# Kernel tuning notes

Measured on AMD Instinct MI355X. Metric: run time of the kernel, lower is better.

The kernel has to match this reference:

```python
import jax, jax.numpy as jnp
import numpy as np

# dims: S slots, B batch, D pred-rep dim, E slot-embedding dim, H hidden/output dim, V per-slot vocab
S, B, D, E, H, V = 7, 4096, 1024, 128, 512, 200
D0 = D + E  # layer-0 LSTM input size


def setup_inputs() -> dict:
    key = jax.random.key(0)
    ks = jax.random.split(key, 12)
    rn = lambda k, shape, s=0.02: jax.random.normal(k, shape, jnp.float32) * s
    return {
        "pred_reps": jax.random.normal(ks[0], (B, D), jnp.float32),
        "slot_labels": jax.random.randint(ks[1], (S, B), 0, V),
        "emb": rn(ks[2], (S, V, E), 1.0),
        # layer 0: per-slot LSTMCell + highway params
        "Wih0": rn(ks[3], (S, 4 * H, D0)), "Whh0": rn(ks[4], (S, 4 * H, H)),
        "bih0": jnp.zeros((S, 4 * H), jnp.float32), "bhh0": jnp.zeros((S, 4 * H), jnp.float32),
        "hwW0": rn(ks[5], (S, H, D0 + H)), "hwb0": jnp.zeros((S, H), jnp.float32),
        "linW0": rn(ks[6], (S, H, D0)),
        # layer 1 (input size = H)
        "Wih1": rn(ks[7], (S, 4 * H, H)), "Whh1": rn(ks[8], (S, 4 * H, H)),
        "bih1": jnp.zeros((S, 4 * H), jnp.float32), "bhh1": jnp.zeros((S, 4 * H), jnp.float32),
        "hwW1": rn(ks[9], (S, H, 2 * H)), "hwb1": jnp.zeros((S, H), jnp.float32),
        "linW1": rn(ks[10], (S, H, H)),
    }


def _lstm_cell(x, h, c, Wih, Whh, bih, bhh):
    # torch LSTMCell: gates ordered i, f, g, o
    gates = x @ Wih.T + bih + h @ Whh.T + bhh
    i, f, g, o = jnp.split(gates, 4, axis=-1)
    c_new = jax.nn.sigmoid(f) * c + jax.nn.sigmoid(i) * jnp.tanh(g)
    h_new = jax.nn.sigmoid(o) * jnp.tanh(c_new)
    return h_new, c_new


def reference(pred_reps, slot_labels, emb, Wih0, Whh0, bih0, bhh0, hwW0, hwb0, linW0,
              Wih1, Whh1, bih1, bhh1, hwW1, hwb1, linW1):
    def step(carry, xs):
        h0, c0, h1, c1 = carry
        (tbl, idx, wih0, whh0, bi0, bh0, hw0, hb0, lw0,
         wih1, whh1, bi1, bh1, hw1, hb1, lw1) = xs
        # per-slot embedding gather + concat with predicate reps  -> [B, D0]
        x = jnp.concatenate([pred_reps, tbl[idx]], axis=-1)
        # layer 0 cell + highway gate
        h0n, c0n = _lstm_cell(x, h0, c0, wih0, whh0, bi0, bh0)
        gate0 = jax.nn.sigmoid(jnp.concatenate([x, h0n], axis=-1) @ hw0.T + hb0)
        x1 = gate0 * h0n + (1.0 - gate0) * (x @ lw0.T)
        # layer 1 cell (its highway output is dead code in the original: curr_input
        # after the last layer is discarded, so we skip it -- same math)
        h1n, c1n = _lstm_cell(x1, h1, c1, wih1, whh1, bi1, bh1)
        return (h0n, c0n, h1n, c1n), None

    init = tuple(jnp.zeros((B, H), pred_reps.dtype) for _ in range(4))
    xs = (emb, slot_labels, Wih0, Whh0, bih0, bhh0, hwW0, hwb0, linW0,
          Wih1, Whh1, bih1, bhh1, hwW1, hwb1, linW1)
    carry, _ = jax.lax.scan(step, init, xs)
    return carry[2]  # last_h: top-layer hidden after final slot
```

## Files before the change

### kernel.cpp

```cpp
#include <hip/hip_runtime.h>
#include <stdint.h>

typedef unsigned short u16;

#define S_   7
#define B_   4096
#define D_   1024
#define E_   128
#define H_   512
#define V_   200
#define D0_  1152
#define K0_  1664
#define KL_  1152
#define KX1  1024
#define G4H  2048
#define XW   2048
#define X1W  2048

typedef __bf16 bf16x8 __attribute__((ext_vector_type(8)));
typedef float  f32x4  __attribute__((ext_vector_type(4)));
typedef u16    u16x8  __attribute__((ext_vector_type(8)));

__device__ __forceinline__ u16 f2bf(float f) {
  union { float f; uint32_t u; } v; v.f = f;
  uint32_t r = v.u + 0x7fffu + ((v.u >> 16) & 1u);
  return (u16)(r >> 16);
}
__device__ __forceinline__ float bf2f(u16 b) {
  union { uint32_t u; float f; } v; v.u = ((uint32_t)b) << 16;
  return v.f;
}
__device__ __forceinline__ float sigmoidf_(float x) { return 1.0f / (1.0f + __expf(-x)); }
__device__ __forceinline__ float tanhf_(float x) {
  float t = __expf(-2.f * fabsf(x));
  return copysignf((1.f - t) / (1.f + t), x);
}

__device__ __forceinline__ void glds16(const u16* g, u16* l) {
  __builtin_amdgcn_global_load_lds(
      (const __attribute__((address_space(1))) uint32_t*)g,
      (__attribute__((address_space(3))) uint32_t*)l, 16, 0, 0);
}

__device__ __forceinline__ void cvt8s(const float* src, u16* dst) {
  const float4* p = (const float4*)src;
  float4 x = p[0], y = p[1];
  u16x8 o;
  o[0]=f2bf(x.x); o[1]=f2bf(x.y); o[2]=f2bf(x.z); o[3]=f2bf(x.w);
  o[4]=f2bf(y.x); o[5]=f2bf(y.y); o[6]=f2bf(y.z); o[7]=f2bf(y.w);
  *(u16x8*)dst = o;
}

__device__ __forceinline__ void pk_gates(const float* __restrict__ Wih,
                                         const float* __restrict__ Whh,
                                         u16* __restrict__ dst,
                                         int idx, int stride, int NG, int KK,
                                         int P1, int P2, int KA, int KB) {
  #pragma unroll
  for (int u = 0; u < 4; ++u) {
    int i = idx + u * stride;
    int r = i / NG, kg = i - r * NG;
    int k8 = kg * 8;
    int g = r >> 9, j = r & 511;
    long drow = (j >> 4) * 64 + g * 16 + (j & 15);
    const float* sp = (k8 < P1) ? Wih + (long)r * KA + k8
                    : (k8 < P2) ? Whh + (long)r * KB + (k8 - P1)
                                : Wih + (long)r * KA + P1 + (k8 - P2);
    cvt8s(sp, &dst[drow * KK + k8]);
  }
}
__device__ __forceinline__ void pk_hwn(const float* __restrict__ src,
                                       u16* __restrict__ dst,
                                       int idx, int stride) {
  #pragma unroll
  for (int u = 0; u < 4; ++u) {
    int i = idx + u * stride;
    int r = i / 208, kg = i - r * 208;
    int k8 = kg * 8;
    const float* sp = (k8 < 1024) ? src + (long)r * K0_ + k8
                    : (k8 < 1536) ? src + (long)r * K0_ + 1152 + (k8 - 1024)
                                  : src + (long)r * K0_ + 1024 + (k8 - 1536);
    cvt8s(sp, &dst[(long)r * K0_ + k8]);
  }
}
__device__ __forceinline__ void pk_lin(const float* __restrict__ src,
                                       u16* __restrict__ dst,
                                       int idx, int stride) {
  #pragma unroll
  for (int u = 0; u < 4; ++u) {
    int i = idx + u * stride;
    int r = i / 144, kg = i - r * 144;
    int k8 = kg * 8;
    cvt8s(src + (long)r * KL_ + k8, &dst[(long)r * KL_ + k8]);
  }
}

__global__ void pack_predz4(const float* __restrict__ pred, u16* __restrict__ dst) {
  const int NG = XW / 8;
  const int stride = gridDim.x * 256;
  int idx = blockIdx.x * 256 + threadIdx.x;
  #pragma unroll
  for (int u = 0; u < 4; ++u) {
    int i = idx + u * stride;
    int row = i / NG, kg = i - row * NG;
    int k8 = kg * 8;
    u16* d = &dst[(long)row * XW + k8];
    if (k8 < 1024) {
      cvt8s(pred + (long)row * D_ + k8, d);
    } else {
      u16x8 z = {};
      *(u16x8*)d = z;
    }
  }
}

__global__ void xgather(const float* __restrict__ emb, const int* __restrict__ labels,
                        u16* __restrict__ EMB) {
  int b = blockIdx.x;
  int e = threadIdx.x;
  #pragma unroll
  for (int s = 0; s < S_; ++s) {
    int ix = labels[s * B_ + b];
    EMB[((long)(s * B_ + b)) * E_ + e] = f2bf(emb[((long)(s * V_ + ix)) * E_ + e]);
  }
}

__global__ void bias_sum(const float* __restrict__ a, const float* __restrict__ b,
                         float* __restrict__ o, int n) {
  int i = blockIdx.x * 256 + threadIdx.x;
  if (i < n) o[i] = a[i] + b[i];
}
__global__ void zero_f(float* __restrict__ p, int n) {
  for (int i = blockIdx.x * 256 + threadIdx.x; i < n; i += gridDim.x * 256) p[i] = 0.f;
}
__global__ void zero_u16k(u16* __restrict__ p, int n) {
  for (int i = blockIdx.x * 256 + threadIdx.x; i < n; i += gridDim.x * 256) p[i] = 0;
}

struct GemmP {
  const u16 *r0, *r1, *r2, *W;
  const float *bsum;
  float *cbuf;
  u16 *hdst;
  float *hf32;
  const u16 *h0src;
  const u16 *xsrc;
  int ld0, ld1, ld2, t1, t2, ldw, nt, ntn, cpx, hld, hoff, h0ld, xld, mode;
};
struct PackP {
  const float *wih0, *whh0, *wih1, *whh1, *hww, *linw;
  u16 *wc0, *wc1, *whn, *wln;
};

__global__ __launch_bounds__(256)
void gemm_multi(GemmP pa, GemmP pb, GemmP pl, GemmP pc, PackP pk,
                int nA, int nAB, int nABL, int nABLC) {
  const int b   = blockIdx.x;
  const int tid = threadIdx.x;

  if (b >= nABLC) {
    int rb = b - nABLC;
    if (rb < 416) {
      pk_gates(pk.wih0, pk.whh0, pk.wc0, rb * 256 + tid, 416 * 256,
               208, K0_, 1024, 1536, D0_, H_);
    } else if (rb < 672) {
      pk_gates(pk.wih1, pk.whh1, pk.wc1, (rb - 416) * 256 + tid, 256 * 256,
               128, KX1, 512, 1024, H_, H_);
    } else if (rb < 776) {
      pk_hwn(pk.hww, pk.whn, (rb - 672) * 256 + tid, 104 * 256);
    } else {
      pk_lin(pk.linw, pk.wln, (rb - 776) * 256 + tid, 72 * 256);
    }
    return;
  }

  __shared__ __align__(16) u16 lds[4 * 8192];
  GemmP P = pc; int base = nABL;
  if (b < nABL) { P = pl; base = nAB; }
  if (b < nAB)  { P = pb; base = nA; }
  if (b < nA)   { P = pa; base = 0; }
  const int bidx = b - base;

  u16* lA = lds;
  u16* lW = lds + 2 * 8192;
  const int lane = tid & 63;
  const int wave = tid >> 6;
  const int bid  = (bidx & 7) * P.cpx + (bidx >> 3);
  const int tn = bid % P.ntn;
  const int tm = bid / P.ntn;
  const long row0 = (long)tm * 128;
  const long col0 = (long)tn * 128;
  const int wm = (wave >> 1) * 64;
  const int wn = (wave & 1) * 64;
  const int fr = lane & 15;
  const int fk = (lane >> 4) * 8;
  const int wr = wave * 32;

  const int srow = wr + (lane >> 3);
  const int scol = ((lane & 7) ^ ((lane >> 3) & 7)) * 8;
  const u16* gr0 = P.r0 + (row0 + srow) * (long)P.ld0 + scol;
  const u16* gr1 = P.r1 + (row0 + srow) * (long)P.ld1 + scol;
  const u16* gr2 = P.r2 + (row0 + srow) * (long)P.ld2 + scol;
  const u16* gw  = P.W  + (col0 + srow) * (long)P.ldw + scol;
  const int dst0 = wr * 64 + lane * 8;

  auto stage = [&](int t, int buf) {
    const u16* g; long ld;
    if (t < P.t1)      { g = gr0 + (long)t * 64;          ld = P.ld0; }
    else if (t < P.t2) { g = gr1 + (long)(t - P.t1) * 64; ld = P.ld1; }
    else               { g = gr2 + (long)(t - P.t2) * 64; ld = P.ld2; }
    const u16* gww = gw + (long)t * 64;
    u16* dA = lA + buf * 8192 + dst0;
    u16* dW = lW + buf * 8192 + dst0;
    #pragma unroll
    for (int i = 0; i < 4; ++i) {
      glds16(g   + (long)(i * 8) * ld,    dA + i * 512);
      glds16(gww + (long)(i * 8) * P.ldw, dW + i * 512);
    }
  };

  int aoff[4], woff[4];
  #pragma unroll
  for (int m = 0; m < 4; ++m) aoff[m] = (wm + m * 16 + fr) * 64;
  #pragma unroll
  for (int n = 0; n < 4; ++n) woff[n] = (wn + n * 16 + fr) * 64;
  const int swz = (fr & 7) << 3;
  const int kk0 = (0 + fk) ^ swz;
  const int kk1 = (32 + fk) ^ swz;

  f32x4 acc[4][4] = {};
  const int nt = P.nt;

  stage(0, 0);

  for (int t = 0; t < nt; ++t) {
    __syncthreads();
    if (t + 1 < nt) stage(t + 1, (t + 1) & 1);
    const u16* Ab = lA + (t & 1) * 8192;
    const u16* Wb = lW + (t & 1) * 8192;
    bf16x8 af0[4], wf0[4], af1[4], wf1[4];
    #pragma unroll
    for (int m = 0; m < 4; ++m) af0[m] = *(const bf16x8*)&Ab[aoff[m] + kk0];
    #pragma unroll
    for (int n = 0; n < 4; ++n) wf0[n] = *(const bf16x8*)&Wb[woff[n] + kk0];
    #pragma unroll
    for (int m = 0; m < 4; ++m) af1[m] = *(const bf16x8*)&Ab[aoff[m] + kk1];
    #pragma unroll
    for (int n = 0; n < 4; ++n) wf1[n] = *(const bf16x8*)&Wb[woff[n] + kk1];
    #pragma unroll
    for (int m = 0; m < 4; ++m)
      #pragma unroll
      for (int n = 0; n < 4; ++n)
        acc[m][n] = __builtin_amdgcn_mfma_f32_16x16x32_bf16(af0[m], wf0[n], acc[m][n], 0, 0, 0);
    #pragma unroll
    for (int m = 0; m < 4; ++m)
      #pragma unroll
      for (int n = 0; n < 4; ++n)
        acc[m][n] = __builtin_amdgcn_mfma_f32_16x16x32_bf16(af1[m], wf1[n], acc[m][n], 0, 0, 0);
  }

  const int cr = (lane >> 4) * 4;
  const int jg = wn >> 6;

  if (P.mode == 0) {
    const int j = tn * 32 + jg * 16 + fr;
    const float bi = P.bsum[j], bf = P.bsum[512 + j];
    const float bg = P.bsum[1024 + j], bo = P.bsum[1536 + j];
    #pragma unroll
    for (int m = 0; m < 4; ++m) {
      const long rbase = row0 + wm + m * 16 + cr;
      #pragma unroll
      for (int r = 0; r < 4; ++r) {
        const long ri = rbase + r;
        float gi = acc[m][0][r] + bi;
        float gf = acc[m][1][r] + bf;
        float gg = acc[m][2][r] + bg;
        float go = acc[m][3][r] + bo;
        float cv = P.cbuf[ri * H_ + j];
        float cn = sigmoidf_(gf) * cv + sigmoidf_(gi) * tanhf_(gg);
        float hn = sigmoidf_(go) * tanhf_(cn);
        P.cbuf[ri * H_ + j] = cn;
        P.hdst[ri * P.hld + P.hoff + j] = f2bf(hn);
        if (P.hf32) P.hf32[ri * H_ + j] = hn;
      }
    }
  } else if (P.mode == 1) {
    #pragma unroll
    for (int n = 0; n < 4; ++n) {
      const int j = (int)(col0) + wn + n * 16 + fr;
      const float bj = P.bsum[j];
      #pragma unroll
      for (int m = 0; m < 4; ++m) {
        const long rbase = row0 + wm + m * 16 + cr;
        #pragma unroll
        for (int r = 0; r < 4; ++r) {
          const long ri = rbase + r;
          float gv = sigmoidf_(acc[m][n][r] + bj);
          float h0 = bf2f(P.h0src[ri * (long)P.h0ld + j]);
          float xl = bf2f(P.xsrc[ri * (long)P.xld + j]);
          float x1 = gv * h0 + (1.f - gv) * xl;
          P.hdst[ri * P.hld + P.hoff + j] = f2bf(x1);
        }
      }
    }
  } else {
    #pragma unroll
    for (int n = 0; n < 4; ++n) {
      const int j = (int)(col0) + wn + n * 16 + fr;
      #pragma unroll
      for (int m = 0; m < 4; ++m) {
        const long rbase = row0 + wm + m * 16 + cr;
        #pragma unroll
        for (int r = 0; r < 4; ++r)
          P.hdst[(rbase + r) * P.hld + P.hoff + j] = f2bf(acc[m][n][r]);
      }
    }
  }
}

extern "C" void kernel_launch(void* const* d_in, const int* in_sizes, int n_in,
                              void* d_out, int out_size, void* d_ws, size_t ws_size,
                              hipStream_t stream) {
  const float* pred   = (const float*)d_in[0];
  const int*   labels = (const int*)d_in[1];
  const float* emb    = (const float*)d_in[2];
  const float* Wih0   = (const float*)d_in[3];
  const float* Whh0   = (const float*)d_in[4];
  const float* bih0   = (const float*)d_in[5];
  const float* bhh0   = (const float*)d_in[6];
  const float* hwW0   = (const float*)d_in[7];
  const float* hwb0   = (const float*)d_in[8];
  const float* linW0  = (const float*)d_in[9];
  const float* Wih1   = (const float*)d_in[10];
  const float* Whh1   = (const float*)d_in[11];
  const float* bih1   = (const float*)d_in[12];
  const float* bhh1   = (const float*)d_in[13];
  float* out = (float*)d_out;

  char* ws = (char*)d_ws;
  size_t off = 0;
  auto alloc = [&](size_t bytes) {
    char* p = ws + off;
    off = (off + bytes + 255) & ~(size_t)255;
    return p;
  };
  u16* WC0  = (u16*)alloc((size_t)S_ * G4H * K0_ * 2);
  u16* WC1  = (u16*)alloc((size_t)S_ * G4H * KX1 * 2);
  u16* HWn  = (u16*)alloc((size_t)S_ * H_ * K0_ * 2);
  u16* LNw  = (u16*)alloc((size_t)S_ * H_ * KL_ * 2);
  u16* xcat = (u16*)alloc((size_t)B_ * XW * 2);
  u16* EMB  = (u16*)alloc((size_t)S_ * B_ * E_ * 2);
  u16* x1cat= (u16*)alloc((size_t)B_ * X1W * 2);
  u16* xlin = (u16*)alloc((size_t)2 * B_ * H_ * 2);
  float* c0  = (float*)alloc((size_t)B_ * H_ * 4);
  float* c1  = (float*)alloc((size_t)B_ * H_ * 4);
  float* bs0 = (float*)alloc((size_t)S_ * G4H * 4);
  float* bs1 = (float*)alloc((size_t)S_ * G4H * 4);

  auto mkPk = [&](int s) {
    PackP K;
    K.wih0 = Wih0 + (size_t)s * G4H * D0_;
    K.whh0 = Whh0 + (size_t)s * G4H * H_;
    K.wih1 = Wih1 + (size_t)s * G4H * H_;
    K.whh1 = Whh1 + (size_t)s * G4H * H_;
    K.hww  = hwW0 + (size_t)s * H_ * K0_;
    K.linw = linW0 + (size_t)s * H_ * KL_;
    K.wc0  = WC0 + (size_t)s * G4H * K0_;
    K.wc1  = WC1 + (size_t)s * G4H * KX1;
    K.whn  = HWn + (size_t)s * H_ * K0_;
    K.wln  = LNw + (size_t)s * H_ * KL_;
    return K;
  };

  GemmP z = {};
  gemm_multi<<<848, 256, 0, stream>>>(z, z, z, z, mkPk(0), 0, 0, 0, 0);
  pack_predz4<<<1024, 256, 0, stream>>>(pred, xcat);
  xgather<<<B_, E_, 0, stream>>>(emb, labels, EMB);
  bias_sum<<<56, 256, 0, stream>>>(bih0, bhh0, bs0, S_ * G4H);
  bias_sum<<<56, 256, 0, stream>>>(bih1, bhh1, bs1, S_ * G4H);
  zero_f<<<256, 256, 0, stream>>>(c0, B_ * H_);
  zero_f<<<256, 256, 0, stream>>>(c1, B_ * H_);
  zero_u16k<<<2048, 256, 0, stream>>>(x1cat, B_ * X1W);

  auto mkA = [&](int s) {
    GemmP P = {};
    P.r0 = xcat;                               P.ld0 = XW;  P.t1 = 16;
    P.r1 = xcat + 1024 + ((s + 1) & 1) * 512;  P.ld1 = XW;  P.t2 = 24;
    P.r2 = EMB + (size_t)s * B_ * E_;          P.ld2 = E_;
    P.W = WC0 + (size_t)s * G4H * K0_;         P.ldw = K0_; P.nt = 26;
    P.ntn = 16; P.cpx = 64;
    P.bsum = bs0 + (size_t)s * G4H; P.cbuf = c0;
    P.hdst = xcat; P.hld = XW; P.hoff = 1024 + (s & 1) * 512;
    P.hf32 = nullptr; P.h0src = xcat; P.h0ld = 0; P.xsrc = xcat; P.xld = 0;
    P.mode = 0;
    return P;
  };
  auto mkB = [&](int s) {
    GemmP P = {};
    P.r0 = xcat;                               P.ld0 = XW;  P.t1 = 16;
    P.r1 = xcat + 1024 + (s & 1) * 512;        P.ld1 = XW;  P.t2 = 24;
    P.r2 = EMB + (size_t)s * B_ * E_;          P.ld2 = E_;
    P.W = HWn + (size_t)s * H_ * K0_;          P.ldw = K0_; P.nt = 26;
    P.ntn = 4; P.cpx = 16;
    P.bsum = hwb0 + (size_t)s * H_; P.cbuf = nullptr;
    P.hdst = x1cat; P.hld = X1W; P.hoff = (s & 1) * 512;
    P.hf32 = nullptr;
    P.h0src = xcat + 1024 + (s & 1) * 512; P.h0ld = XW;
    P.xsrc = xlin + (size_t)(s & 1) * B_ * H_; P.xld = H_;
    P.mode = 1;
    return P;
  };
  auto mkL = [&](int s) {
    GemmP P = {};
    P.r0 = xcat;                               P.ld0 = XW;  P.t1 = 16;
    P.r1 = xcat;                               P.ld1 = XW;  P.t2 = 16;
    P.r2 = EMB + (size_t)s * B_ * E_;          P.ld2 = E_;
    P.W = LNw + (size_t)s * H_ * KL_;          P.ldw = KL_; P.nt = 18;
    P.ntn = 4; P.cpx = 16;
    P.bsum = hwb0; P.cbuf = nullptr;
    P.hdst = xlin + (size_t)(s & 1) * B_ * H_; P.hld = H_; P.hoff = 0;
    P.hf32 = nullptr; P.h0src = xcat; P.h0ld = 0; P.xsrc = xcat; P.xld = 0;
    P.mode = 2;
    return P;
  };
  auto mkC = [&](int s) {
    GemmP P = {};
    P.r0 = x1cat + (s & 1) * 512;              P.ld0 = X1W; P.t1 = 8;
    P.r1 = x1cat + 1024 + ((s + 1) & 1) * 512; P.ld1 = X1W; P.t2 = 16;
    P.r2 = P.r0;                               P.ld2 = X1W;
    P.W = WC1 + (size_t)s * G4H * KX1;         P.ldw = KX1; P.nt = 16;
    P.ntn = 16; P.cpx = 64;
    P.bsum = bs1 + (size_t)s * G4H; P.cbuf = c1;
    P.hdst = x1cat; P.hld = X1W; P.hoff = 1024 + (s & 1) * 512;
    P.hf32 = (s == 6) ? out : nullptr; P.h0src = x1cat; P.h0ld = 0;
    P.xsrc = x1cat; P.xld = 0;
    P.mode = 0;
    return P;
  };

  for (int k = 0; k <= 8; ++k) {
    const int nA = (k <= 6) ? 512 : 0;
    const int nB = (k >= 1 && k <= 7) ? 128 : 0;
    const int nL = (k <= 6) ? 128 : 0;
    const int nC = (k >= 2) ? 512 : 0;
    const int nD = (k <= 5) ? 848 : 0;
    GemmP pa, pb, pl, pc;
    if (nA) pa = mkA(k);
    if (nB) pb = mkB(k - 1);
    if (nL) pl = mkL(k);
    if (nC) pc = mkC(k - 2);
    GemmP any = nA ? pa : (nB ? pb : (nL ? pl : pc));
    if (!nA) pa = any;
    if (!nB) pb = any;
    if (!nL) pl = any;
    if (!nC) pc = any;
    PackP pk = mkPk(nD ? (k + 1) : 0);
    gemm_multi<<<nA + nB + nL + nC + nD, 256, 0, stream>>>(
        pa, pb, pl, pc, pk, nA, nA + nB, nA + nB + nL, nA + nB + nL + nC);
  }
}
```

Before: 630.9 us.

## Enlarge GEMM tiles to 256x256 with 512 threads and triple-buffered weight pipeline

Grows each workgroup's output tile from 128x128 to 256x256 using 8 waves (512 threads) with a K-step of 32. Weight tiles are triple-buffered and prefetched two steps ahead, with explicit waitcnt/barrier control and raised priority around the MFMA block. The aim is higher operand reuse and better overlap of global-to-LDS loads with compute. In exchange, grids become four times smaller (fewer workgroups for 256 CUs), register pressure rises with 32 accumulators per lane, and LDS use grows.

```diff
diff --git a/kernel.cpp b/kernel.cpp
--- a/kernel.cpp
+++ b/kernel.cpp
@@ -152,7 +152,7 @@
   u16 *wc0, *wc1, *whn, *wln;
 };
 
-__global__ __launch_bounds__(256)
+__global__ __launch_bounds__(512, 2)
 void gemm_multi(GemmP pa, GemmP pb, GemmP pl, GemmP pc, PackP pk,
                 int nA, int nAB, int nABL, int nABLC) {
   const int b   = blockIdx.x;
@@ -160,115 +160,127 @@
 
   if (b >= nABLC) {
     int rb = b - nABLC;
-    if (rb < 416) {
-      pk_gates(pk.wih0, pk.whh0, pk.wc0, rb * 256 + tid, 416 * 256,
+    if (rb < 208) {
+      pk_gates(pk.wih0, pk.whh0, pk.wc0, rb * 512 + tid, 208 * 512,
                208, K0_, 1024, 1536, D0_, H_);
-    } else if (rb < 672) {
-      pk_gates(pk.wih1, pk.whh1, pk.wc1, (rb - 416) * 256 + tid, 256 * 256,
+    } else if (rb < 336) {
+      pk_gates(pk.wih1, pk.whh1, pk.wc1, (rb - 208) * 512 + tid, 128 * 512,
                128, KX1, 512, 1024, H_, H_);
-    } else if (rb < 776) {
-      pk_hwn(pk.hww, pk.whn, (rb - 672) * 256 + tid, 104 * 256);
+    } else if (rb < 388) {
+      pk_hwn(pk.hww, pk.whn, (rb - 336) * 512 + tid, 52 * 512);
     } else {
-      pk_lin(pk.linw, pk.wln, (rb - 776) * 256 + tid, 72 * 256);
+      pk_lin(pk.linw, pk.wln, (rb - 388) * 512 + tid, 36 * 512);
     }
     return;
   }
 
-  __shared__ __align__(16) u16 lds[4 * 8192];
+  __shared__ __align__(16) u16 lds[5 * 8192];
+  u16* lA = lds;
+  u16* lW = lds + 2 * 8192;
+
   GemmP P = pc; int base = nABL;
   if (b < nABL) { P = pl; base = nAB; }
   if (b < nAB)  { P = pb; base = nA; }
   if (b < nA)   { P = pa; base = 0; }
   const int bidx = b - base;
 
-  u16* lA = lds;
-  u16* lW = lds + 2 * 8192;
   const int lane = tid & 63;
   const int wave = tid >> 6;
   const int bid  = (bidx & 7) * P.cpx + (bidx >> 3);
   const int tn = bid % P.ntn;
   const int tm = bid / P.ntn;
-  const long row0 = (long)tm * 128;
-  const long col0 = (long)tn * 128;
-  const int wm = (wave >> 1) * 64;
-  const int wn = (wave & 1) * 64;
+  const long row0 = (long)tm * 256;
+  const long col0 = (long)tn * 256;
   const int fr = lane & 15;
-  const int fk = (lane >> 4) * 8;
-  const int wr = wave * 32;
-
-  const int srow = wr + (lane >> 3);
-  const int scol = ((lane & 7) ^ ((lane >> 3) & 7)) * 8;
-  const u16* gr0 = P.r0 + (row0 + srow) * (long)P.ld0 + scol;
-  const u16* gr1 = P.r1 + (row0 + srow) * (long)P.ld1 + scol;
-  const u16* gr2 = P.r2 + (row0 + srow) * (long)P.ld2 + scol;
-  const u16* gw  = P.W  + (col0 + srow) * (long)P.ldw + scol;
-  const int dst0 = wr * 64 + lane * 8;
-
-  auto stage = [&](int t, int buf) {
+  const int ks = lane >> 4;
+
+  const int segL = (tid & 7) ^ ((tid >> 3) & 7);
+  const int srow = (tid >> 3) + (segL >> 2) * 128;
+  const int ksg  = (segL & 3) * 8;
+  const u16* ga0 = P.r0 + (row0 + srow) * (long)P.ld0 + ksg;
+  const u16* ga1 = P.r1 + (row0 + srow) * (long)P.ld1 + ksg;
+  const u16* ga2 = P.r2 + (row0 + srow) * (long)P.ld2 + ksg;
+  const u16* gww = P.W  + (col0 + srow) * (long)P.ldw + ksg;
+  const int dst0 = tid * 8;
+
+  auto stageA = [&](int t, int buf) {
     const u16* g; long ld;
-    if (t < P.t1)      { g = gr0 + (long)t * 64;          ld = P.ld0; }
-    else if (t < P.t2) { g = gr1 + (long)(t - P.t1) * 64; ld = P.ld1; }
-    else               { g = gr2 + (long)(t - P.t2) * 64; ld = P.ld2; }
-    const u16* gww = gw + (long)t * 64;
-    u16* dA = lA + buf * 8192 + dst0;
-    u16* dW = lW + buf * 8192 + dst0;
-    #pragma unroll
-    for (int i = 0; i < 4; ++i) {
-      glds16(g   + (long)(i * 8) * ld,    dA + i * 512);
-      glds16(gww + (long)(i * 8) * P.ldw, dW + i * 512);
-    }
-  };
-
-  int aoff[4], woff[4];
-  #pragma unroll
-  for (int m = 0; m < 4; ++m) aoff[m] = (wm + m * 16 + fr) * 64;
-  #pragma unroll
-  for (int n = 0; n < 4; ++n) woff[n] = (wn + n * 16 + fr) * 64;
-  const int swz = (fr & 7) << 3;
-  const int kk0 = (0 + fk) ^ swz;
-  const int kk1 = (32 + fk) ^ swz;
-
-  f32x4 acc[4][4] = {};
+    if (t < P.t1)      { g = ga0 + (long)t * 32;          ld = P.ld0; }
+    else if (t < P.t2) { g = ga1 + (long)(t - P.t1) * 32; ld = P.ld1; }
+    else               { g = ga2 + (long)(t - P.t2) * 32; ld = P.ld2; }
+    u16* d = lA + buf * 8192 + dst0;
+    glds16(g,               d);
+    glds16(g + 64 * ld,     d + 4096);
+  };
+  auto stageW = [&](int t, int buf) {
+    const u16* g = gww + (long)t * 32;
+    u16* d = lW + buf * 8192 + dst0;
+    glds16(g,                       d);
+    glds16(g + 64 * (long)P.ldw,    d + 4096);
+  };
+
+  const int segA = (wave >> 2) * 4 + ks;
+  const int segW = ((wave & 3) >> 1) * 4 + ks;
+  const int wnl  = (wave & 1) * 64;
+  int aoff[8], woff[4];
+  #pragma unroll
+  for (int m = 0; m < 8; ++m)
+    aoff[m] = (m * 16 + fr) * 64 + ((segA ^ (fr & 7)) * 8);
+  #pragma unroll
+  for (int n = 0; n < 4; ++n)
+    woff[n] = (wnl + n * 16 + fr) * 64 + ((segW ^ (fr & 7)) * 8);
+
+  f32x4 acc[8][4] = {};
   const int nt = P.nt;
 
-  stage(0, 0);
-
+  stageA(0, 0);
+  stageW(0, 0);
+  stageW(1, 1);
+  asm volatile("s_waitcnt vmcnt(2)" ::: "memory");
+  __builtin_amdgcn_s_barrier();
+
+  int wrd = 0;
   for (int t = 0; t < nt; ++t) {
-    __syncthreads();
-    if (t + 1 < nt) stage(t + 1, (t + 1) & 1);
     const u16* Ab = lA + (t & 1) * 8192;
-    const u16* Wb = lW + (t & 1) * 8192;
-    bf16x8 af0[4], wf0[4], af1[4], wf1[4];
-    #pragma unroll
-    for (int m = 0; m < 4; ++m) af0[m] = *(const bf16x8*)&Ab[aoff[m] + kk0];
-    #pragma unroll
-    for (int n = 0; n < 4; ++n) wf0[n] = *(const bf16x8*)&Wb[woff[n] + kk0];
-    #pragma unroll
-    for (int m = 0; m < 4; ++m) af1[m] = *(const bf16x8*)&Ab[aoff[m] + kk1];
-    #pragma unroll
-    for (int n = 0; n < 4; ++n) wf1[n] = *(const bf16x8*)&Wb[woff[n] + kk1];
-    #pragma unroll
-    for (int m = 0; m < 4; ++m)
+    const u16* Wb = lW + wrd * 8192;
+    bf16x8 af[8], wf[4];
+    #pragma unroll
+    for (int m = 0; m < 8; ++m) af[m] = *(const bf16x8*)&Ab[aoff[m]];
+    #pragma unroll
+    for (int n = 0; n < 4; ++n) wf[n] = *(const bf16x8*)&Wb[woff[n]];
+
+    if (t + 1 < nt) stageA(t + 1, (t + 1) & 1);
+    const int ws2 = (wrd >= 1) ? wrd - 1 : 2;
+    if (t + 2 < nt) stageW(t + 2, ws2);
+
+    asm volatile("s_waitcnt lgkmcnt(0)" ::: "memory");
+    __builtin_amdgcn_sched_barrier(0);
+    __builtin_amdgcn_s_setprio(1);
+    #pragma unroll
+    for (int m = 0; m < 8; ++m)
       #pragma unroll
       for (int n = 0; n < 4; ++n)
-        acc[m][n] = __builtin_amdgcn_mfma_f32_16x16x32_bf16(af0[m], wf0[n], acc[m][n], 0, 0, 0);
-    #pragma unroll
-    for (int m = 0; m < 4; ++m)
-      #pragma unroll
-      for (int n = 0; n < 4; ++n)
-        acc[m][n] = __builtin_amdgcn_mfma_f32_16x16x32_bf16(af1[m], wf1[n], acc[m][n], 0, 0, 0);
+        acc[m][n] = __builtin_amdgcn_mfma_f32_16x16x32_bf16(af[m], wf[n], acc[m][n], 0, 0, 0);
+    __builtin_amdgcn_s_setprio(0);
+
+    if (t + 1 < nt) {
+      if (t + 2 < nt) asm volatile("s_waitcnt vmcnt(2)" ::: "memory");
+      else            asm volatile("s_waitcnt vmcnt(0)" ::: "memory");
+      __builtin_amdgcn_s_barrier();
+    }
+    wrd = (wrd == 2) ? 0 : wrd + 1;
   }
 
   const int cr = (lane >> 4) * 4;
-  const int jg = wn >> 6;
+  const long rwm = row0 + (wave >> 2) * 128;
 
   if (P.mode == 0) {
-    const int j = tn * 32 + jg * 16 + fr;
+    const int j = (tn * 4 + (wave & 3)) * 16 + fr;
     const float bi = P.bsum[j], bf = P.bsum[512 + j];
     const float bg = P.bsum[1024 + j], bo = P.bsum[1536 + j];
     #pragma unroll
-    for (int m = 0; m < 4; ++m) {
-      const long rbase = row0 + wm + m * 16 + cr;
+    for (int m = 0; m < 8; ++m) {
+      const long rbase = rwm + m * 16 + cr;
       #pragma unroll
       for (int r = 0; r < 4; ++r) {
         const long ri = rbase + r;
@@ -287,11 +299,11 @@
   } else if (P.mode == 1) {
     #pragma unroll
     for (int n = 0; n < 4; ++n) {
-      const int j = (int)(col0) + wn + n * 16 + fr;
+      const int j = (int)col0 + (wave & 3) * 64 + n * 16 + fr;
       const float bj = P.bsum[j];
       #pragma unroll
-      for (int m = 0; m < 4; ++m) {
-        const long rbase = row0 + wm + m * 16 + cr;
+      for (int m = 0; m < 8; ++m) {
+        const long rbase = rwm + m * 16 + cr;
         #pragma unroll
         for (int r = 0; r < 4; ++r) {
           const long ri = rbase + r;
@@ -306,10 +318,10 @@
   } else {
     #pragma unroll
     for (int n = 0; n < 4; ++n) {
-      const int j = (int)(col0) + wn + n * 16 + fr;
+      const int j = (int)col0 + (wave & 3) * 64 + n * 16 + fr;
       #pragma unroll
-      for (int m = 0; m < 4; ++m) {
-        const long rbase = row0 + wm + m * 16 + cr;
+      for (int m = 0; m < 8; ++m) {
+        const long rbase = rwm + m * 16 + cr;
         #pragma unroll
         for (int r = 0; r < 4; ++r)
           P.hdst[(rbase + r) * P.hld + P.hoff + j] = f2bf(acc[m][n][r]);
@@ -373,7 +385,7 @@
   };
 
   GemmP z = {};
-  gemm_multi<<<848, 256, 0, stream>>>(z, z, z, z, mkPk(0), 0, 0, 0, 0);
+  gemm_multi<<<424, 512, 0, stream>>>(z, z, z, z, mkPk(0), 0, 0, 0, 0);
   pack_predz4<<<1024, 256, 0, stream>>>(pred, xcat);
   xgather<<<B_, E_, 0, stream>>>(emb, labels, EMB);
   bias_sum<<<56, 256, 0, stream>>>(bih0, bhh0, bs0, S_ * G4H);
@@ -384,11 +396,11 @@
 
   auto mkA = [&](int s) {
     GemmP P = {};
-    P.r0 = xcat;                               P.ld0 = XW;  P.t1 = 16;
-    P.r1 = xcat + 1024 + ((s + 1) & 1) * 512;  P.ld1 = XW;  P.t2 = 24;
+    P.r0 = xcat;                               P.ld0 = XW;  P.t1 = 32;
+    P.r1 = xcat + 1024 + ((s + 1) & 1) * 512;  P.ld1 = XW;  P.t2 = 48;
     P.r2 = EMB + (size_t)s * B_ * E_;          P.ld2 = E_;
-    P.W = WC0 + (size_t)s * G4H * K0_;         P.ldw = K0_; P.nt = 26;
-    P.ntn = 16; P.cpx = 64;
+    P.W = WC0 + (size_t)s * G4H * K0_;         P.ldw = K0_; P.nt = 52;
+    P.ntn = 8; P.cpx = 16;
     P.bsum = bs0 + (size_t)s * G4H; P.cbuf = c0;
     P.hdst = xcat; P.hld = XW; P.hoff = 1024 + (s & 1) * 512;
     P.hf32 = nullptr; P.h0src = xcat; P.h0ld = 0; P.xsrc = xcat; P.xld = 0;
@@ -397,11 +409,11 @@
   };
   auto mkB = [&](int s) {
     GemmP P = {};
-    P.r0 = xcat;                               P.ld0 = XW;  P.t1 = 16;
-    P.r1 = xcat + 1024 + (s & 1) * 512;        P.ld1 = XW;  P.t2 = 24;
+    P.r0 = xcat;                               P.ld0 = XW;  P.t1 = 32;
+    P.r1 = xcat + 1024 + (s & 1) * 512;        P.ld1 = XW;  P.t2 = 48;
     P.r2 = EMB + (size_t)s * B_ * E_;          P.ld2 = E_;
-    P.W = HWn + (size_t)s * H_ * K0_;          P.ldw = K0_; P.nt = 26;
-    P.ntn = 4; P.cpx = 16;
+    P.W = HWn + (size_t)s * H_ * K0_;          P.ldw = K0_; P.nt = 52;
+    P.ntn = 2; P.cpx = 4;
     P.bsum = hwb0 + (size_t)s * H_; P.cbuf = nullptr;
     P.hdst = x1cat; P.hld = X1W; P.hoff = (s & 1) * 512;
     P.hf32 = nullptr;
@@ -412,11 +424,11 @@
   };
   auto mkL = [&](int s) {
     GemmP P = {};
-    P.r0 = xcat;                               P.ld0 = XW;  P.t1 = 16;
-    P.r1 = xcat;                               P.ld1 = XW;  P.t2 = 16;
+    P.r0 = xcat;                               P.ld0 = XW;  P.t1 = 32;
+    P.r1 = xcat;                               P.ld1 = XW;  P.t2 = 32;
     P.r2 = EMB + (size_t)s * B_ * E_;          P.ld2 = E_;
-    P.W = LNw + (size_t)s * H_ * KL_;          P.ldw = KL_; P.nt = 18;
-    P.ntn = 4; P.cpx = 16;
+    P.W = LNw + (size_t)s * H_ * KL_;          P.ldw = KL_; P.nt = 36;
+    P.ntn = 2; P.cpx = 4;
     P.bsum = hwb0; P.cbuf = nullptr;
     P.hdst = xlin + (size_t)(s & 1) * B_ * H_; P.hld = H_; P.hoff = 0;
     P.hf32 = nullptr; P.h0src = xcat; P.h0ld = 0; P.xsrc = xcat; P.xld = 0;
@@ -425,11 +437,11 @@
   };
   auto mkC = [&](int s) {
     GemmP P = {};
-    P.r0 = x1cat + (s & 1) * 512;              P.ld0 = X1W; P.t1 = 8;
-    P.r1 = x1cat + 1024 + ((s + 1) & 1) * 512; P.ld1 = X1W; P.t2 = 16;
+    P.r0 = x1cat + (s & 1) * 512;              P.ld0 = X1W; P.t1 = 16;
+    P.r1 = x1cat + 1024 + ((s + 1) & 1) * 512; P.ld1 = X1W; P.t2 = 32;
     P.r2 = P.r0;                               P.ld2 = X1W;
-    P.W = WC1 + (size_t)s * G4H * KX1;         P.ldw = KX1; P.nt = 16;
-    P.ntn = 16; P.cpx = 64;
+    P.W = WC1 + (size_t)s * G4H * KX1;         P.ldw = KX1; P.nt = 32;
+    P.ntn = 8; P.cpx = 16;
     P.bsum = bs1 + (size_t)s * G4H; P.cbuf = c1;
     P.hdst = x1cat; P.hld = X1W; P.hoff = 1024 + (s & 1) * 512;
     P.hf32 = (s == 6) ? out : nullptr; P.h0src = x1cat; P.h0ld = 0;
@@ -439,11 +451,11 @@
   };
 
   for (int k = 0; k <= 8; ++k) {
-    const int nA = (k <= 6) ? 512 : 0;
-    const int nB = (k >= 1 && k <= 7) ? 128 : 0;
-    const int nL = (k <= 6) ? 128 : 0;
-    const int nC = (k >= 2) ? 512 : 0;
-    const int nD = (k <= 5) ? 848 : 0;
+    const int nA = (k <= 6) ? 128 : 0;
+    const int nB = (k >= 1 && k <= 7) ? 32 : 0;
+    const int nL = (k <= 6) ? 32 : 0;
+    const int nC = (k >= 2) ? 128 : 0;
+    const int nD = (k <= 5) ? 424 : 0;
     GemmP pa, pb, pl, pc;
     if (nA) pa = mkA(k);
     if (nB) pb = mkB(k - 1);
@@ -455,7 +467,7 @@
     if (!nL) pl = any;
     if (!nC) pc = any;
     PackP pk = mkPk(nD ? (k + 1) : 0);
-    gemm_multi<<<nA + nB + nL + nC + nD, 256, 0, stream>>>(
+    gemm_multi<<<nA + nB + nL + nC + nD, 512, 0, stream>>>(
         pa, pb, pl, pc, pk, nA, nA + nB, nA + nB + nL, nA + nB + nL + nC);
   }
 }
```

New measurement: 904.5 us. +43.4%, slower.
